# Kernel tuning notes

Measured on AMD Instinct MI355X. Metric: run time of the kernel, lower is better.

## Reference

```python
import jax, jax.numpy as jnp
import numpy as np

B, N, I, O, CG, H, E = 32, 256, 16, 16, 64, 64, 4096
SEQ_LEN = 256  # sequence_length init arg (temporal attention scale)


def setup_inputs() -> dict:
    key = jax.random.key(0)
    ks = jax.random.split(key, 24)
    r = lambda i, shape, s: jax.random.normal(ks[i], shape, jnp.float32) * s
    return {
        'data': jax.random.normal(ks[0], (B, I, N), jnp.float32),
        'masks': jax.random.bernoulli(ks[1], 0.8, (B, I, N)),
        'edge_index': jax.random.randint(ks[2], (2, E), 0, N, jnp.int64),
        'gcn_w': r(3, (I, CG), 0.2),
        'gcn_b': jnp.zeros((CG,), jnp.float32),
        'sa_qw': r(4, (CG, CG), 0.1), 'sa_qb': jnp.zeros((CG,), jnp.float32),
        'sa_kw': r(5, (CG, CG), 0.1), 'sa_kb': jnp.zeros((CG,), jnp.float32),
        'gru_wih': r(6, (3 * H, I), 0.1), 'gru_whh': r(7, (3 * H, H), 0.1),
        'gru_bih': jnp.zeros((3 * H,), jnp.float32), 'gru_bhh': jnp.zeros((3 * H,), jnp.float32),
        'ta_qw': r(8, (H, H), 0.1), 'ta_qb': jnp.zeros((H,), jnp.float32),
        'ta_kw': r(9, (H, H), 0.1), 'ta_kb': jnp.zeros((H,), jnp.float32),
        'fc1_w': r(10, (H * N * 2, H * N // 4), 0.005), 'fc1_b': jnp.zeros((H * N // 4,), jnp.float32),
        'fc2_w': r(11, (H * N // 4, O * N), 0.01), 'fc2_b': jnp.zeros((O * N,), jnp.float32),
    }


def _forward(data, masks, edge_index, gcn_w, gcn_b, sa_qw, sa_qb, sa_kw, sa_kb,
             gru_wih, gru_whh, gru_bih, gru_bhh, ta_qw, ta_qb, ta_kw, ta_kb,
             fc1_w, fc1_b, fc2_w, fc2_b):
    data = jnp.where(masks, data, 0.0)            # [B, I, N]
    x = jnp.swapaxes(data, 1, 2)                  # [B, N, I] (per-sample node features)

    loop = jnp.arange(N)
    src = jnp.concatenate([edge_index[0], loop])
    dst = jnp.concatenate([edge_index[1], loop])
    w = jnp.concatenate([jnp.ones((E,), jnp.float32), 2.0 * jnp.ones((N,), jnp.float32)])
    deg = jax.ops.segment_sum(w, dst, num_segments=N)
    dinv = jnp.where(deg > 0, jax.lax.rsqrt(deg), 0.0)
    norm = dinv[src] * w * dinv[dst]              # [E+N]
    xw = x @ gcn_w                                # [B, N, CG]
    msg = xw[:, src, :] * norm[None, :, None]     # gather + scale
    agg = jax.vmap(lambda m: jax.ops.segment_sum(m, dst, num_segments=N))(msg)
    h = jax.nn.relu(agg + gcn_b)                  # [B, N, CG]

    # --- SpatialAttention (per sample, scale 1/sqrt(num_nodes)) ---
    q = h @ sa_qw + sa_qb
    k = h @ sa_kw + sa_kb
    att = jax.nn.softmax(jnp.einsum('bnc,bmc->bnm', q, k) / np.sqrt(N).astype(np.float32), axis=-1)
    ha = jnp.einsum('bnm,bmc->bnc', att, h)

    # torch stacks x.T -> [B, CG, N] then .view(B, -1, CG): a reshape, not a transpose
    se = jnp.swapaxes(h, 1, 2).reshape(B, N, CG)
    sa = jnp.swapaxes(ha, 1, 2).reshape(B, N, CG)
    # dropout is identity in eval mode

    # --- GRU (1 layer, batch_first) over rnn_input = data.view(B, -1, I) ---
    rnn_in = data.reshape(B, N, I)
    def step(hprev, xt):
        gi = xt @ gru_wih.T + gru_bih
        gh = hprev @ gru_whh.T + gru_bhh
        ir, iz, inn = jnp.split(gi, 3, axis=-1)
        hr, hz, hn = jnp.split(gh, 3, axis=-1)
        r = jax.nn.sigmoid(ir + hr)
        z = jax.nn.sigmoid(iz + hz)
        n = jnp.tanh(inn + r * hn)
        hnew = (1.0 - z) * n + z * hprev
        return hnew, hnew
    h0 = jnp.zeros((B, H), jnp.float32)
    _, outs = jax.lax.scan(step, h0, jnp.swapaxes(rnn_in, 0, 1))
    rnn_out = jnp.swapaxes(outs, 0, 1)            # [B, N, H]

    # --- TemporalAttention (scale 1/sqrt(sequence_length)) ---
    qt = rnn_out @ ta_qw + ta_qb
    kt = rnn_out @ ta_kw + ta_kb
    att_t = jax.nn.softmax(jnp.einsum('btc,bsc->bts', qt, kt) / np.sqrt(SEQ_LEN).astype(np.float32), axis=-1)
    rnn_a = jnp.einsum('bts,bsc->btc', att_t, rnn_out)

    # --- fused MLP combine ---
    embed = jnp.concatenate([rnn_out, se], axis=-1).reshape(B, -1)  # [B, 2*H*N]
    inter = embed @ fc1_w + fc1_b
    final = inter @ fc2_w + fc2_b
    final = jnp.swapaxes(final.reshape(B, N, O), 1, 2)              # [B, O, N]
    rnn_a = jnp.swapaxes(rnn_a, 1, 2)                               # [B, H, N]
    return final, sa, rnn_a


def reference(data, masks, edge_index, gcn_w, gcn_b, sa_qw, sa_qb, sa_kw, sa_kb,
              gru_wih, gru_whh, gru_bih, gru_bhh, ta_qw, ta_qb, ta_kw, ta_kb,
              fc1_w, fc1_b, fc2_w, fc2_b):
    return _forward(data, masks, edge_index, gcn_w, gcn_b, sa_qw, sa_qb, sa_kw, sa_kb,
                    gru_wih, gru_whh, gru_bih, gru_bhh, ta_qw, ta_qb, ta_kw, ta_kb,
                    fc1_w, fc1_b, fc2_w, fc2_b)
```

## Files before the change

kernel.cpp:

```cpp
#include <hip/hip_runtime.h>

#define NB 32
#define NN 256
#define NI 16
#define NO 16
#define NC 64
#define NH 64
#define NE 4096
#define FC1_N 4096

__device__ __forceinline__ float sigmoidf_(float x){ return 1.0f/(1.0f+__expf(-x)); }
__device__ __forceinline__ float tanhf_(float x){
  float e = __expf(2.0f*x);
  return 1.0f - 2.0f/(e+1.0f);
}

__device__ __forceinline__ void gload16(const void* g, void* l){
  __builtin_amdgcn_global_load_lds((const __attribute__((address_space(1))) void*)g,
                                   (__attribute__((address_space(3))) void*)l, 16, 0, 0);
}

__global__ void k_detect(const unsigned char* __restrict__ m8, const int* __restrict__ ei, int* flags){
  int t = blockIdx.x*256 + threadIdx.x;
  unsigned a = (unsigned)m8[t*4+1] | (unsigned)m8[t*4+2] | (unsigned)m8[t*4+3];
  if (__any(a != 0) && (threadIdx.x & 63) == 0) atomicOr(&flags[0], 1);
  unsigned b = 0;
  if (t < 4096) b = (unsigned)ei[2*t+1];
  if (__any(b != 0) && (threadIdx.x & 63) == 0) atomicOr(&flags[1], 1);
}

__global__ void k_mask(const float* __restrict__ data, const unsigned char* __restrict__ m8,
                       const int* __restrict__ flags, float* __restrict__ dm){
  int i = blockIdx.x*256 + threadIdx.x;
  int mv = flags[0] ? (int)m8[i] : ((const int*)m8)[i];
  dm[i] = mv ? data[i] : 0.0f;
}

__device__ __forceinline__ int edge_src(const int* ei, const int* flags, int e){
  return flags[1] ? ei[e] : ei[2*e];
}
__device__ __forceinline__ int edge_dst(const int* ei, const int* flags, int e){
  return flags[1] ? ei[NE + e] : ei[2*(NE + e)];
}

__global__ __launch_bounds__(256) void k_graph(const int* __restrict__ ei, const int* __restrict__ flags,
                                               float* wadj){
  int t = threadIdx.x;
  float4 z = {0.f,0.f,0.f,0.f};
  for (int x = t; x < 16384; x += 256) ((float4*)wadj)[x] = z;
  __shared__ float degs[NN];
  __shared__ float dls[NN];
  degs[t] = 0.f;
  __syncthreads();
  for (int e = t; e < NE; e += 256) atomicAdd(&degs[edge_dst(ei, flags, e)], 1.0f);
  __syncthreads();
  float di = rsqrtf(degs[t] + 2.0f);
  dls[t] = di;
  atomicAdd(&wadj[t*NN + t], 2.0f*di*di);
  __syncthreads();
  for (int e = t; e < NE; e += 256){
    int s = edge_src(ei, flags, e), d = edge_dst(ei, flags, e);
    atomicAdd(&wadj[d*NN + s], dls[s]*dls[d]);
  }
}

__global__ void k_xw(const float* __restrict__ dm, const float* __restrict__ gw, float* __restrict__ xw){
  int idx = blockIdx.x*256 + threadIdx.x;
  int c = idx & 63, n = (idx>>6) & 255, b = idx>>14;
  const float* dmb = dm + b*NI*NN;
  float a = 0.f;
  #pragma unroll
  for (int i=0;i<NI;i++) a += dmb[i*NN + n]*gw[i*NC + c];
  xw[idx] = a;
}

__global__ void k_agg(const float* __restrict__ wadj, const float* __restrict__ xw,
                      const float* __restrict__ gb, float* __restrict__ h){
  int idx = blockIdx.x*256 + threadIdx.x;
  int c = idx & 63, n = (idx>>6) & 255, b = idx>>14;
  const float* wr = wadj + n*NN;
  const float* xb = xw + b*NN*NC + c;
  float a = gb[c];
  #pragma unroll 4
  for (int m=0;m<NN;m++) a += wr[m]*xb[m*NC];
  h[idx] = fmaxf(a, 0.0f);
}

__global__ void k_qk2(const float* __restrict__ hb, const float* __restrict__ rnn,
    const float* __restrict__ saqw, const float* __restrict__ saqb,
    const float* __restrict__ sakw, const float* __restrict__ sakb,
    const float* __restrict__ taqw, const float* __restrict__ taqb,
    const float* __restrict__ takw, const float* __restrict__ takb,
    float* __restrict__ qb, float* __restrict__ kb, float* __restrict__ qt, float* __restrict__ kt){
  int bid = blockIdx.x;
  const float *src, *qw, *qbias, *kw, *kbias; float *qo, *ko;
  if (bid < 2048){ src=hb; qw=saqw; qbias=saqb; kw=sakw; kbias=sakb; qo=qb; ko=kb; }
  else { bid -= 2048; src=rnn; qw=taqw; qbias=taqb; kw=takw; kbias=takb; qo=qt; ko=kt; }
  int idx = bid*256 + threadIdx.x;
  int c = idx & 63;
  const float* hr = src + (idx>>6)*NC;
  float aq = qbias[c], ak = kbias[c];
  #pragma unroll 8
  for (int cc=0; cc<NC; cc++){ float hv = hr[cc]; aq += hv*qw[cc*NC + c]; ak += hv*kw[cc*NC + c]; }
  qo[idx] = aq; ko[idx] = ak;
}

__global__ __launch_bounds__(256) void k_attn2(const float* __restrict__ qb, const float* __restrict__ kb,
    const float* __restrict__ hb, const float* __restrict__ qt, const float* __restrict__ kt,
    const float* __restrict__ rnn, float* __restrict__ out_sa, float* __restrict__ out_ra){
  int bidx = blockIdx.x;
  const float *q, *kmat, *v; float* outp;
  if (bidx < 1024){ q=qb; kmat=kb; v=hb; outp=out_sa; }
  else { bidx -= 1024; q=qt; kmat=kt; v=rnn; outp=out_ra; }
  int b = bidx >> 5, n0 = (bidx & 31)*8;
  int t = threadIdx.x;
  const float scale = 0.0625f;
  __shared__ __align__(16) float qs[8][64];
  __shared__ float S[8][256];
  #pragma unroll
  for (int rep=0; rep<2; rep++){
    int j = rep*256 + t; int r = j>>6, c = j&63;
    qs[r][c] = q[((b<<8) + n0 + r)*NC + c];
  }
  __syncthreads();
  float4 kr[16];
  const float4* kp = (const float4*)(kmat + ((b<<8) + t)*NC);
  #pragma unroll
  for (int i=0;i<16;i++) kr[i] = kp[i];
  #pragma unroll
  for (int r=0;r<8;r++){
    const float4* q4 = (const float4*)qs[r];
    float s = 0.f;
    #pragma unroll
    for (int i=0;i<16;i++){ float4 a=q4[i], bb=kr[i]; s += a.x*bb.x + a.y*bb.y + a.z*bb.z + a.w*bb.w; }
    S[r][t] = s*scale;
  }
  __syncthreads();
  {
    int g = t>>5, l = t&31;
    float vals[8];
    #pragma unroll
    for (int k2=0;k2<8;k2++) vals[k2] = S[g][l + (k2<<5)];
    float mx = vals[0];
    #pragma unroll
    for (int k2=1;k2<8;k2++) mx = fmaxf(mx, vals[k2]);
    #pragma unroll
    for (int off=16; off; off>>=1) mx = fmaxf(mx, __shfl_xor(mx, off));
    float sm = 0.f;
    #pragma unroll
    for (int k2=0;k2<8;k2++){ vals[k2] = __expf(vals[k2]-mx); sm += vals[k2]; }
    #pragma unroll
    for (int off=16; off; off>>=1) sm += __shfl_xor(sm, off);
    float rS = 1.0f/sm;
    #pragma unroll
    for (int k2=0;k2<8;k2++) S[g][l + (k2<<5)] = vals[k2]*rS;
  }
  __syncthreads();
  int c = t & 63, rp = t >> 6;
  const float* vp = v + (b<<8)*NC + c;
  float a0 = 0.f, a1 = 0.f;
  #pragma unroll 4
  for (int m=0;m<NN;m++){
    float vv = vp[m*NC];
    a0 += S[rp][m]*vv;
    a1 += S[rp+4][m]*vv;
  }
  outp[(((b<<6)+c)<<8) + n0 + rp]     = a0;
  outp[(((b<<6)+c)<<8) + n0 + rp + 4] = a1;
}

__global__ __launch_bounds__(192) void k_gru(const float* __restrict__ dm,
        const float* __restrict__ wih, const float* __restrict__ bih,
        const float* __restrict__ whh, const float* __restrict__ bhh,
        float* __restrict__ rnn){
  int b = blockIdx.x, j = threadIdx.x;
  __shared__ __align__(16) float dmS[4096];
  __shared__ __align__(16) float hs[64];
  __shared__ float gh[192];
  __shared__ float gin[64];
  float wh[64];
  const float4* wr = (const float4*)(whh + j*NH);
  #pragma unroll
  for (int k4=0;k4<16;k4++){ float4 t4 = wr[k4]; wh[4*k4]=t4.x; wh[4*k4+1]=t4.y; wh[4*k4+2]=t4.z; wh[4*k4+3]=t4.w; }
  float wi[16];
  const float4* wir = (const float4*)(wih + j*NI);
  #pragma unroll
  for (int k4=0;k4<4;k4++){ float4 t4 = wir[k4]; wi[4*k4]=t4.x; wi[4*k4+1]=t4.y; wi[4*k4+2]=t4.z; wi[4*k4+3]=t4.w; }
  float bj = bhh[j], bij = bih[j];
  const float4* dmb4 = (const float4*)(dm + b*4096);
  for (int x = j; x < 1024; x += 192) ((float4*)dmS)[x] = dmb4[x];
  if (j < 64) hs[j] = 0.f;
  __syncthreads();
  for (int t=0;t<NN;t++){
    const float* xt = &dmS[t*16];
    float gival = bij;
    #pragma unroll
    for (int i=0;i<16;i++) gival += wi[i]*xt[i];
    float a0=0.f,a1=0.f,a2=0.f,a3=0.f;
    #pragma unroll
    for (int k4=0;k4<16;k4++){
      float4 hv = *(const float4*)&hs[4*k4];
      a0 += wh[4*k4+0]*hv.x; a1 += wh[4*k4+1]*hv.y; a2 += wh[4*k4+2]*hv.z; a3 += wh[4*k4+3]*hv.w;
    }
    float ghv = a0+a1+a2+a3+bj;
    if (j < 128) gh[j] = ghv + gival;
    else { gh[j] = ghv; gin[j-128] = gival; }
    __syncthreads();
    if (j < 64){
      float r  = sigmoidf_(gh[j]);
      float z  = sigmoidf_(gh[j+64]);
      float nn = tanhf_   (gin[j] + r*gh[j+128]);
      float hn = nn + z*(hs[j]-nn);
      rnn[(b*NN + t)*NH + j] = hn;
      hs[j] = hn;
    }
    __syncthreads();
  }
}

__global__ void k_embedT(const float* __restrict__ rnn, const float* __restrict__ h,
                         float* __restrict__ ET){
  int idx = blockIdx.x*256 + threadIdx.x;
  int bb = idx & 31, rr = idx >> 5;
  int n = rr >> 7, c = rr & 127;
  float v;
  if (c < 64) v = rnn[((bb<<8) + n)*NH + c];
  else { int f = (n<<6) + (c-64); v = h[(bb<<14) + ((f&255)<<6) + (f>>8)]; }
  ET[idx] = v;
}

template<int KC>
__global__ __launch_bounds__(512, 4) void k_fc(const float* __restrict__ W,
        const float* __restrict__ Ein, float* __restrict__ part){
  const int tid = threadIdx.x, lane = tid & 63, wv_ = tid >> 6;
  const int cw = wv_ & 1, bq = wv_ >> 1;
  const int c0 = blockIdx.x*512;
  const long k0 = (long)blockIdx.y*KC;
  __shared__ __align__(16) float wlds[2][8][512];
  __shared__ __align__(16) float elds[2][256];
  float acc[4][8];
  #pragma unroll
  for (int c=0;c<4;c++)
    #pragma unroll
    for (int bb=0;bb<8;bb++) acc[c][bb]=0.f;

  const int NCH = KC/8;
  #define STAGE_FC(ch, bf) { \
    const float* wsrc = W + (k0 + (long)(ch)*8)*FC1_N + c0; \
    gload16(wsrc + (long)wv_*FC1_N + lane*4,       &wlds[bf][wv_][0]); \
    gload16(wsrc + (long)wv_*FC1_N + 256 + lane*4, &wlds[bf][wv_][256]); \
    if (wv_ == 0) gload16(Ein + (k0 + (long)(ch)*8)*32 + lane*4, &elds[bf][0]); \
  }

  STAGE_FC(0, 0)
  int cur = 0;
  for (int ch=0; ch<NCH; ch++){
    __syncthreads();
    if (ch+1 < NCH) STAGE_FC(ch+1, cur^1)
    #pragma unroll
    for (int r=0;r<8;r++){
      float4 wv4 = *(const float4*)&wlds[cur][r][cw*256 + lane*4];
      float4 e0 = *(const float4*)&elds[cur][r*32 + bq*8];
      float4 e1 = *(const float4*)&elds[cur][r*32 + bq*8 + 4];
      float ev[8] = {e0.x,e0.y,e0.z,e0.w,e1.x,e1.y,e1.z,e1.w};
      #pragma unroll
      for (int bb=0;bb<8;bb++){
        acc[0][bb] += wv4.x*ev[bb];
        acc[1][bb] += wv4.y*ev[bb];
        acc[2][bb] += wv4.z*ev[bb];
        acc[3][bb] += wv4.w*ev[bb];
      }
    }
    cur ^= 1;
  }
  float* pp = part + (long)blockIdx.y*131072 + (long)(bq*8)*FC1_N + c0 + cw*256 + lane*4;
  #pragma unroll
  for (int bb=0;bb<8;bb++){
    float4 o; o.x=acc[0][bb]; o.y=acc[1][bb]; o.z=acc[2][bb]; o.w=acc[3][bb];
    *(float4*)(pp + (long)bb*FC1_N) = o;
  }
  #undef STAGE_FC
}

__global__ void k_red1(const float* __restrict__ part, const float* __restrict__ bias,
                       float* __restrict__ ITr){
  int idx = blockIdx.x*256 + threadIdx.x;
  int b = idx >> 12, col = idx & 4095;
  float a = bias[col];
  #pragma unroll 16
  for (int y=0;y<64;y++) a += part[(long)y*131072 + b*FC1_N + col];
  ITr[col*32 + b] = a;
}

__global__ void k_red2(const float* __restrict__ part, const float* __restrict__ bias,
                       float* __restrict__ outp){
  int idx = blockIdx.x*256 + threadIdx.x;
  int b = idx >> 12, col = idx & 4095;
  float a = bias[col];
  #pragma unroll 16
  for (int y=0;y<64;y++) a += part[(long)y*131072 + b*FC1_N + col];
  int n = col >> 4, o = col & 15;
  outp[(b<<12) + (o<<8) + n] = a;
}

extern "C" void kernel_launch(void* const* d_in, const int* in_sizes, int n_in,
                              void* d_out, int out_size, void* d_ws, size_t ws_size,
                              hipStream_t stream) {
  const float* data   = (const float*)d_in[0];
  const unsigned char* masks = (const unsigned char*)d_in[1];
  const int* ei       = (const int*)d_in[2];
  const float* gcn_w  = (const float*)d_in[3];
  const float* gcn_b  = (const float*)d_in[4];
  const float* sa_qw  = (const float*)d_in[5];
  const float* sa_qb  = (const float*)d_in[6];
  const float* sa_kw  = (const float*)d_in[7];
  const float* sa_kb  = (const float*)d_in[8];
  const float* wih    = (const float*)d_in[9];
  const float* whh    = (const float*)d_in[10];
  const float* bih    = (const float*)d_in[11];
  const float* bhh    = (const float*)d_in[12];
  const float* ta_qw  = (const float*)d_in[13];
  const float* ta_qb  = (const float*)d_in[14];
  const float* ta_kw  = (const float*)d_in[15];
  const float* ta_kb  = (const float*)d_in[16];
  const float* fc1_w  = (const float*)d_in[17];
  const float* fc1_b  = (const float*)d_in[18];
  const float* fc2_w  = (const float*)d_in[19];
  const float* fc2_b  = (const float*)d_in[20];

  float* dm    = (float*)d_ws;
  float* wadj  = dm + 131072;
  int*   flags = (int*)(wadj + 65536);
  float* xw    = (float*)(flags + 8);
  float* hb    = xw + 524288;
  float* qb    = hb + 524288;
  float* kb    = qb + 524288;
  float* rnn   = kb + 524288;
  float* qt    = rnn + 524288;
  float* kt    = qt + 524288;
  float* ET    = kt + 524288;
  float* ITr   = ET + 1048576;
  float* part1 = ITr + 131072;
  float* part2 = part1 + 64*131072;

  float* out_final = (float*)d_out;
  float* out_sa = out_final + 131072;
  float* out_ra = out_final + 655360;

  hipMemsetAsync(flags, 0, 32, stream);

  k_detect<<<128,256,0,stream>>>(masks, ei, flags);
  k_mask<<<512,256,0,stream>>>(data, masks, flags, dm);
  k_graph<<<1,256,0,stream>>>(ei, flags, wadj);
  k_xw<<<2048,256,0,stream>>>(dm, gcn_w, xw);
  k_gru<<<32,192,0,stream>>>(dm, wih, bih, whh, bhh, rnn);
  k_agg<<<2048,256,0,stream>>>(wadj, xw, gcn_b, hb);
  k_qk2<<<4096,256,0,stream>>>(hb, rnn, sa_qw, sa_qb, sa_kw, sa_kb,
                               ta_qw, ta_qb, ta_kw, ta_kb, qb, kb, qt, kt);
  k_attn2<<<2048,256,0,stream>>>(qb, kb, hb, qt, kt, rnn, out_sa, out_ra);
  k_embedT<<<4096,256,0,stream>>>(rnn, hb, ET);
  { dim3 g(8,64); k_fc<512><<<g,512,0,stream>>>(fc1_w, ET, part1); }
  k_red1<<<512,256,0,stream>>>(part1, fc1_b, ITr);
  { dim3 g(8,64); k_fc<64><<<g,512,0,stream>>>(fc2_w, ITr, part2); }
  k_red2<<<512,256,0,stream>>>(part2, fc2_b, out_final);
}
```

Before: 504.3 us.

## Widen FC column tiles, read activations from global, vectorize split-K reductions

The FC GEMV-like kernel now covers 1024 output columns per block, with each thread holding 2x8 float4 accumulators. Activation vectors are read directly from global memory (cached) instead of being staged in LDS. FC1 split-K doubles to 128 chunks of 256 rows, which doubles the partial-sum buffer. The reduction kernels now use float4 loads, with each thread handling four columns. The change is meant to raise arithmetic intensity per weight load and cut reduction memory traffic, at the cost of more registers and more partial-sum writes for FC1.

```diff
diff --git a/kernel.cpp b/kernel.cpp
--- a/kernel.cpp
+++ b/kernel.cpp
@@ -232,75 +232,99 @@
 template<int KC>
 __global__ __launch_bounds__(512, 4) void k_fc(const float* __restrict__ W,
         const float* __restrict__ Ein, float* __restrict__ part){
+  __shared__ __align__(16) float wlds[2][8][1024];
   const int tid = threadIdx.x, lane = tid & 63, wv_ = tid >> 6;
   const int cw = wv_ & 1, bq = wv_ >> 1;
-  const int c0 = blockIdx.x*512;
+  const int c0 = blockIdx.x*1024;
   const long k0 = (long)blockIdx.y*KC;
-  __shared__ __align__(16) float wlds[2][8][512];
-  __shared__ __align__(16) float elds[2][256];
-  float acc[4][8];
-  #pragma unroll
-  for (int c=0;c<4;c++)
-    #pragma unroll
-    for (int bb=0;bb<8;bb++) acc[c][bb]=0.f;
+  float4 acc[2][8];
+  #pragma unroll
+  for (int q=0;q<2;q++)
+    #pragma unroll
+    for (int j=0;j<8;j++) acc[q][j] = (float4){0.f,0.f,0.f,0.f};
 
   const int NCH = KC/8;
   #define STAGE_FC(ch, bf) { \
-    const float* wsrc = W + (k0 + (long)(ch)*8)*FC1_N + c0; \
-    gload16(wsrc + (long)wv_*FC1_N + lane*4,       &wlds[bf][wv_][0]); \
-    gload16(wsrc + (long)wv_*FC1_N + 256 + lane*4, &wlds[bf][wv_][256]); \
-    if (wv_ == 0) gload16(Ein + (k0 + (long)(ch)*8)*32 + lane*4, &elds[bf][0]); \
+    const float* wsrc = W + (k0 + (long)(ch)*8 + wv_)*FC1_N + c0; \
+    gload16(wsrc + lane*4,       &wlds[bf][wv_][0]); \
+    gload16(wsrc + 256 + lane*4, &wlds[bf][wv_][256]); \
+    gload16(wsrc + 512 + lane*4, &wlds[bf][wv_][512]); \
+    gload16(wsrc + 768 + lane*4, &wlds[bf][wv_][768]); \
   }
 
   STAGE_FC(0, 0)
-  int cur = 0;
   for (int ch=0; ch<NCH; ch++){
+    const int cur = ch & 1;
     __syncthreads();
     if (ch+1 < NCH) STAGE_FC(ch+1, cur^1)
+    const float* ep = Ein + (k0 + (long)ch*8)*32 + bq*8;
     #pragma unroll
     for (int r=0;r<8;r++){
-      float4 wv4 = *(const float4*)&wlds[cur][r][cw*256 + lane*4];
-      float4 e0 = *(const float4*)&elds[cur][r*32 + bq*8];
-      float4 e1 = *(const float4*)&elds[cur][r*32 + bq*8 + 4];
-      float ev[8] = {e0.x,e0.y,e0.z,e0.w,e1.x,e1.y,e1.z,e1.w};
-      #pragma unroll
-      for (int bb=0;bb<8;bb++){
-        acc[0][bb] += wv4.x*ev[bb];
-        acc[1][bb] += wv4.y*ev[bb];
-        acc[2][bb] += wv4.z*ev[bb];
-        acc[3][bb] += wv4.w*ev[bb];
-      }
+      float4 w0 = *(const float4*)&wlds[cur][r][cw*512 + lane*4];
+      float4 w1 = *(const float4*)&wlds[cur][r][cw*512 + 256 + lane*4];
+      float4 e0 = *(const float4*)(ep + r*32);
+      float4 e1 = *(const float4*)(ep + r*32 + 4);
+      acc[0][0].x+=w0.x*e0.x; acc[0][0].y+=w0.y*e0.x; acc[0][0].z+=w0.z*e0.x; acc[0][0].w+=w0.w*e0.x;
+      acc[1][0].x+=w1.x*e0.x; acc[1][0].y+=w1.y*e0.x; acc[1][0].z+=w1.z*e0.x; acc[1][0].w+=w1.w*e0.x;
+      acc[0][1].x+=w0.x*e0.y; acc[0][1].y+=w0.y*e0.y; acc[0][1].z+=w0.z*e0.y; acc[0][1].w+=w0.w*e0.y;
+      acc[1][1].x+=w1.x*e0.y; acc[1][1].y+=w1.y*e0.y; acc[1][1].z+=w1.z*e0.y; acc[1][1].w+=w1.w*e0.y;
+      acc[0][2].x+=w0.x*e0.z; acc[0][2].y+=w0.y*e0.z; acc[0][2].z+=w0.z*e0.z; acc[0][2].w+=w0.w*e0.z;
+      acc[1][2].x+=w1.x*e0.z; acc[1][2].y+=w1.y*e0.z; acc[1][2].z+=w1.z*e0.z; acc[1][2].w+=w1.w*e0.z;
+      acc[0][3].x+=w0.x*e0.w; acc[0][3].y+=w0.y*e0.w; acc[0][3].z+=w0.z*e0.w; acc[0][3].w+=w0.w*e0.w;
+      acc[1][3].x+=w1.x*e0.w; acc[1][3].y+=w1.y*e0.w; acc[1][3].z+=w1.z*e0.w; acc[1][3].w+=w1.w*e0.w;
+      acc[0][4].x+=w0.x*e1.x; acc[0][4].y+=w0.y*e1.x; acc[0][4].z+=w0.z*e1.x; acc[0][4].w+=w0.w*e1.x;
+      acc[1][4].x+=w1.x*e1.x; acc[1][4].y+=w1.y*e1.x; acc[1][4].z+=w1.z*e1.x; acc[1][4].w+=w1.w*e1.x;
+      acc[0][5].x+=w0.x*e1.y; acc[0][5].y+=w0.y*e1.y; acc[0][5].z+=w0.z*e1.y; acc[0][5].w+=w0.w*e1.y;
+      acc[1][5].x+=w1.x*e1.y; acc[1][5].y+=w1.y*e1.y; acc[1][5].z+=w1.z*e1.y; acc[1][5].w+=w1.w*e1.y;
+      acc[0][6].x+=w0.x*e1.z; acc[0][6].y+=w0.y*e1.z; acc[0][6].z+=w0.z*e1.z; acc[0][6].w+=w0.w*e1.z;
+      acc[1][6].x+=w1.x*e1.z; acc[1][6].y+=w1.y*e1.z; acc[1][6].z+=w1.z*e1.z; acc[1][6].w+=w1.w*e1.z;
+      acc[0][7].x+=w0.x*e1.w; acc[0][7].y+=w0.y*e1.w; acc[0][7].z+=w0.z*e1.w; acc[0][7].w+=w0.w*e1.w;
+      acc[1][7].x+=w1.x*e1.w; acc[1][7].y+=w1.y*e1.w; acc[1][7].z+=w1.z*e1.w; acc[1][7].w+=w1.w*e1.w;
     }
-    cur ^= 1;
-  }
-  float* pp = part + (long)blockIdx.y*131072 + (long)(bq*8)*FC1_N + c0 + cw*256 + lane*4;
-  #pragma unroll
-  for (int bb=0;bb<8;bb++){
-    float4 o; o.x=acc[0][bb]; o.y=acc[1][bb]; o.z=acc[2][bb]; o.w=acc[3][bb];
-    *(float4*)(pp + (long)bb*FC1_N) = o;
+  }
+  float* pp = part + (long)blockIdx.y*131072 + (long)(bq*8)*FC1_N + c0 + cw*512 + lane*4;
+  #pragma unroll
+  for (int j=0;j<8;j++){
+    *(float4*)(pp + (long)j*FC1_N)       = acc[0][j];
+    *(float4*)(pp + (long)j*FC1_N + 256) = acc[1][j];
   }
   #undef STAGE_FC
 }
 
 __global__ void k_red1(const float* __restrict__ part, const float* __restrict__ bias,
                        float* __restrict__ ITr){
-  int idx = blockIdx.x*256 + threadIdx.x;
-  int b = idx >> 12, col = idx & 4095;
-  float a = bias[col];
+  int idx4 = blockIdx.x*256 + threadIdx.x;
+  int b = idx4 >> 10, col4 = idx4 & 1023;
+  float4 a = ((const float4*)bias)[col4];
   #pragma unroll 16
-  for (int y=0;y<64;y++) a += part[(long)y*131072 + b*FC1_N + col];
-  ITr[col*32 + b] = a;
+  for (int y=0;y<128;y++){
+    float4 p = ((const float4*)(part + (long)y*131072 + (long)b*FC1_N))[col4];
+    a.x+=p.x; a.y+=p.y; a.z+=p.z; a.w+=p.w;
+  }
+  int col = col4*4;
+  ITr[(col+0)*32 + b] = a.x;
+  ITr[(col+1)*32 + b] = a.y;
+  ITr[(col+2)*32 + b] = a.z;
+  ITr[(col+3)*32 + b] = a.w;
 }
 
 __global__ void k_red2(const float* __restrict__ part, const float* __restrict__ bias,
                        float* __restrict__ outp){
-  int idx = blockIdx.x*256 + threadIdx.x;
-  int b = idx >> 12, col = idx & 4095;
-  float a = bias[col];
+  int idx4 = blockIdx.x*256 + threadIdx.x;
+  int b = idx4 >> 10, col4 = idx4 & 1023;
+  float4 a = ((const float4*)bias)[col4];
   #pragma unroll 16
-  for (int y=0;y<64;y++) a += part[(long)y*131072 + b*FC1_N + col];
-  int n = col >> 4, o = col & 15;
-  outp[(b<<12) + (o<<8) + n] = a;
+  for (int y=0;y<64;y++){
+    float4 p = ((const float4*)(part + (long)y*131072 + (long)b*FC1_N))[col4];
+    a.x+=p.x; a.y+=p.y; a.z+=p.z; a.w+=p.w;
+  }
+  float av[4] = {a.x, a.y, a.z, a.w};
+  #pragma unroll
+  for (int c=0;c<4;c++){
+    int col = col4*4 + c;
+    int n = col >> 4, o = col & 15;
+    outp[(b<<12) + (o<<8) + n] = av[c];
+  }
 }
 
 extern "C" void kernel_launch(void* const* d_in, const int* in_sizes, int n_in,
@@ -341,7 +365,7 @@
   float* ET    = kt + 524288;
   float* ITr   = ET + 1048576;
   float* part1 = ITr + 131072;
-  float* part2 = part1 + 64*131072;
+  float* part2 = part1 + 128*131072;
 
   float* out_final = (float*)d_out;
   float* out_sa = out_final + 131072;
@@ -359,8 +383,8 @@
                                ta_qw, ta_qb, ta_kw, ta_kb, qb, kb, qt, kt);
   k_attn2<<<2048,256,0,stream>>>(qb, kb, hb, qt, kt, rnn, out_sa, out_ra);
   k_embedT<<<4096,256,0,stream>>>(rnn, hb, ET);
-  { dim3 g(8,64); k_fc<512><<<g,512,0,stream>>>(fc1_w, ET, part1); }
-  k_red1<<<512,256,0,stream>>>(part1, fc1_b, ITr);
-  { dim3 g(8,64); k_fc<64><<<g,512,0,stream>>>(fc2_w, ITr, part2); }
-  k_red2<<<512,256,0,stream>>>(part2, fc2_b, out_final);
-}
+  { dim3 g(4,128); k_fc<256><<<g,512,0,stream>>>(fc1_w, ET, part1); }
+  k_red1<<<128,256,0,stream>>>(part1, fc1_b, ITr);
+  { dim3 g(4,64); k_fc<64><<<g,512,0,stream>>>(fc2_w, ITr, part2); }
+  k_red2<<<128,256,0,stream>>>(part2, fc2_b, out_final);
+}
```

Result: slower. 559.3 us (+10.9%).
